# Kernel tuning notes

Measured on AMD Instinct MI355X. Metric: run time of the kernel, lower is better.

The kernel has to match this reference:

```python
import jax, jax.numpy as jnp
import numpy as np
from jax import lax


def conv2d(x, w, stride=1, padding=0, dilation=1, bias=None):
    s = (stride, stride) if isinstance(stride, int) else stride
    p = (padding, padding) if isinstance(padding, int) else padding
    d = (dilation, dilation) if isinstance(dilation, int) else dilation
    out = lax.conv_general_dilated(x, w, s, [(p[0], p[0]), (p[1], p[1])],
                                   rhs_dilation=d,
                                   dimension_numbers=('NCHW', 'OIHW', 'NCHW'))
    if bias is not None:
        out = out + bias[None, :, None, None]
    return out


def bn(x, eps=1e-5):
    # BatchNorm2d in training mode with default affine params (gamma=1, beta=0)
    m = x.mean((0, 2, 3), keepdims=True)
    v = jnp.mean((x - m) ** 2, (0, 2, 3), keepdims=True)
    return (x - m) * lax.rsqrt(v + eps)


def cbam(x, w_fc1, w_fc2, w_sp):
    mlp = lambda v: conv2d(jax.nn.relu(conv2d(v, w_fc1)), w_fc2)
    ca = jax.nn.sigmoid(mlp(x.mean((2, 3), keepdims=True)) + mlp(x.max((2, 3), keepdims=True)))
    x = x * ca
    sp = jnp.concatenate([x.mean(1, keepdims=True), x.max(1, keepdims=True)], 1)
    return x * jax.nn.sigmoid(conv2d(sp, w_sp, padding=3))


def deform_conv(x, offset, w_kernel, ks=3, padding=1):
    b, c, h, w = x.shape
    N = ks * ks
    # reorder interleaved offsets -> all x-offsets then all y-offsets
    reorder = jnp.concatenate([jnp.arange(0, 2 * N, 2), jnp.arange(1, 2 * N, 2)])
    offset = offset[:, reorder]
    xp = jnp.pad(x, ((0, 0), (0, 0), (padding, padding), (padding, padding)))
    Hp, Wp = h + 2 * padding, w + 2 * padding
    r = jnp.arange(-(ks - 1) // 2, (ks - 1) // 2 + 1)
    knx, kny = jnp.meshgrid(r, r, indexing='ij')
    p_n = jnp.concatenate([knx.ravel(), kny.ravel()]).astype(x.dtype).reshape(1, 2 * N, 1, 1)
    gx, gy = jnp.meshgrid(jnp.arange(1, h + 1), jnp.arange(1, w + 1), indexing='ij')
    p_0 = jnp.concatenate([jnp.broadcast_to(gx[None, None], (1, N, h, w)),
                           jnp.broadcast_to(gy[None, None], (1, N, h, w))], 1).astype(x.dtype)
    p = jnp.transpose(p_0 + p_n + offset, (0, 2, 3, 1))  # [b,h,w,2N]
    clampq = lambda q: jnp.concatenate([jnp.clip(q[..., :N], 0, Hp - 1),
                                        jnp.clip(q[..., N:], 0, Wp - 1)], -1)
    fl = jnp.floor(lax.stop_gradient(p))
    q_lt = clampq(fl).astype(jnp.int32)
    q_rb = clampq(fl + 1).astype(jnp.int32)
    q_lb = jnp.concatenate([q_lt[..., :N], q_rb[..., N:]], -1)
    q_rt = jnp.concatenate([q_rb[..., :N], q_lt[..., N:]], -1)
    mask = jnp.concatenate([(p[..., :N] < padding) | (p[..., :N] > Hp - 1 - padding),
                            (p[..., N:] < padding) | (p[..., N:] > Wp - 1 - padding)], -1)
    mask = lax.stop_gradient(mask.astype(p.dtype))
    # floor_p = p - (p - floor(p)) carries zero gradient in the original
    p = p * (1 - mask) + lax.stop_gradient(jnp.floor(p)) * mask
    p = clampq(p)
    px, py = p[..., :N], p[..., N:]
    def g(q, sx, sy):
        return ((1 + sx * (q[..., :N].astype(p.dtype) - px)) *
                (1 + sy * (q[..., N:].astype(p.dtype) - py)))
    xf = xp.reshape(b, c, Hp * Wp)
    def gather(q):
        idx = (q[..., :N] * Wp + q[..., N:]).reshape(b, 1, h * w * N)
        v = jnp.take_along_axis(xf, jnp.broadcast_to(idx, (b, c, h * w * N)), axis=2)
        return v.reshape(b, c, h, w, N)
    xo = (g(q_lt, 1, 1)[:, None] * gather(q_lt) + g(q_rb, -1, -1)[:, None] * gather(q_rb)
          + g(q_lb, 1, -1)[:, None] * gather(q_lb) + g(q_rt, -1, 1)[:, None] * gather(q_rt))
    # [b,c,h,w,N] -> [b,c,h*ks,w*ks] (N = kernel_row*ks + kernel_col)
    xo = xo.reshape(b, c, h, w, ks, ks).transpose(0, 1, 2, 4, 3, 5).reshape(b, c, h * ks, w * ks)
    return conv2d(xo, w_kernel, stride=ks)


def _forward(lf, hf, w_conv1_1, b_conv1_1, w_conv, w_offset, b_offset, w_deform,
             w_dil1, w_dil2, w_dil3, w_dil4, w_conv1, w_conv2,
             w_fc1, w_fc2, w_sp, w_conv1_2, b_conv1_2, w_conv3_3):
    hf = jax.nn.relu(bn(conv2d(hf, w_conv1_1, bias=b_conv1_1)))  # Conv1x1
    xc = jnp.split(lf, 4, axis=1)
    def branch(prev, extra, w_dil, dil):
        x = bn(conv2d(jnp.concatenate([prev, hf], 1), w_conv, padding=1))
        t = x + extra
        off = conv2d(t, w_offset, padding=1, bias=b_offset)
        d = deform_conv(t, off, w_deform)
        d = bn(conv2d(d, w_dil, padding=dil, dilation=dil))
        d = bn(conv2d(d, w_conv1, padding=1))
        d = cbam(d, w_fc1, w_fc2, w_sp)
        return bn(conv2d(d, w_conv2, padding=1))
    x0_1 = branch(xc[0], xc[1], w_dil1, 1)
    x1_2 = branch(x0_1, x0_1 + xc[2], w_dil2, 2)
    x2_3 = branch(x1_2, x1_2 + xc[3], w_dil3, 3)
    x3_4 = branch(x2_3, x2_3, w_dil4, 4)
    xx = jax.nn.relu(bn(conv2d(jnp.concatenate([x0_1, x1_2, x2_3, x3_4], 1),
                               w_conv1_2, bias=b_conv1_2)))
    return bn(conv2d(lf + xx, w_conv3_3, padding=1))


def setup_inputs() -> dict:
    key = jax.random.key(0)
    ks = jax.random.split(key, 20)
    B, C, H, W = 4, 64, 256, 256
    c4 = C // 4
    rn = lambda k, shp, s=0.05: jax.random.normal(k, shp, dtype=jnp.float32) * s
    return {
        'lf': rn(ks[0], (B, C, H, W), 1.0),
        'hf': rn(ks[1], (B, C, H, W), 1.0),
        'w_conv1_1': rn(ks[2], (c4, C, 1, 1)),
        'b_conv1_1': jnp.zeros((c4,), jnp.float32),
        'w_conv': rn(ks[3], (c4, C // 2, 3, 3)),
        'w_offset': rn(ks[4], (18, c4, 3, 3)),
        'b_offset': jnp.zeros((18,), jnp.float32),
        'w_deform': rn(ks[5], (c4, c4, 3, 3)),
        'w_dil1': rn(ks[6], (c4, c4, 3, 3)),
        'w_dil2': rn(ks[7], (c4, c4, 3, 3)),
        'w_dil3': rn(ks[8], (c4, c4, 3, 3)),
        'w_dil4': rn(ks[9], (c4, c4, 3, 3)),
        'w_conv1': rn(ks[10], (C, c4, 3, 3)),
        'w_conv2': rn(ks[11], (c4, C, 3, 3)),
        'w_fc1': rn(ks[12], (C // 16, C, 1, 1)),
        'w_fc2': rn(ks[13], (C, C // 16, 1, 1)),
        'w_sp': rn(ks[14], (1, 2, 7, 7)),
        'w_conv1_2': rn(ks[15], (C, C, 1, 1)),
        'b_conv1_2': jnp.zeros((C,), jnp.float32),
        'w_conv3_3': rn(ks[16], (C, C, 3, 3)),
    }


def reference(lf, hf, w_conv1_1, b_conv1_1, w_conv, w_offset, b_offset, w_deform,
              w_dil1, w_dil2, w_dil3, w_dil4, w_conv1, w_conv2,
              w_fc1, w_fc2, w_sp, w_conv1_2, b_conv1_2, w_conv3_3):
    return _forward(lf, hf, w_conv1_1, b_conv1_1, w_conv, w_offset, b_offset, w_deform,
                    w_dil1, w_dil2, w_dil3, w_dil4, w_conv1, w_conv2,
                    w_fc1, w_fc2, w_sp, w_conv1_2, b_conv1_2, w_conv3_3)
```

## Files before the change

kernel.cpp:

```cpp
#include <hip/hip_runtime.h>
#include <math.h>

#define HW 65536
#define Wd 256
#define Hd 256
#define Bn 4
#define NS 16

template<int CIN1,int CIN2,int COUT,int COB,int DIL>
__global__ __launch_bounds__(256) void conv3_k(
    const float* __restrict__ inA, long long a_bs,
    const float* __restrict__ inB,
    const float* __restrict__ add_in,
    const float* __restrict__ w, const float* __restrict__ bias,
    const float* __restrict__ scale_c, const float* __restrict__ scale_p,
    float* __restrict__ out)
{
    constexpr int CIN = CIN1 + CIN2;
    constexpr int SP = 2*DIL + 4;
    int tx = threadIdx.x & 15, ty = threadIdx.x >> 4;
    int j0 = blockIdx.x*64 + tx*4;
    int iy = blockIdx.y & 15;
    int chunk = blockIdx.y >> 4;
    int i = iy*16 + ty;
    int b = blockIdx.z;
    int o0 = chunk*COB;

    float acc[COB][4];
#pragma unroll
    for(int o=0;o<COB;o++){
        float bv = bias ? bias[o0+o] : 0.f;
#pragma unroll
        for(int q=0;q<4;q++) acc[o][q] = bv;
    }

    const float* spb = scale_p ? scale_p + (size_t)b*HW : nullptr;

    for(int c=0;c<CIN;c++){
        const float* cb;
        if (CIN2 == 0 || c < CIN1) cb = inA + (size_t)b*a_bs + (size_t)c*HW;
        else                       cb = inB + ((size_t)b*CIN2 + (c-CIN1))*HW;
        const float* ab = add_in ? add_in + (size_t)b*a_bs + (size_t)c*HW : nullptr;
        float sc = scale_c ? scale_c[b*CIN + c] : 1.f;

        float r[3][SP];
#pragma unroll
        for(int kh=0;kh<3;kh++){
#pragma unroll
            for(int t=0;t<SP;t++) r[kh][t] = 0.f;
            int ii = i + (kh-1)*DIL;
            if (ii < 0 || ii >= Hd) continue;
            const float* row = cb + ii*Wd;
            float4 c4 = *(const float4*)(row + j0);
            r[kh][DIL+0]=c4.x; r[kh][DIL+1]=c4.y; r[kh][DIL+2]=c4.z; r[kh][DIL+3]=c4.w;
#pragma unroll
            for(int t=0;t<DIL;t++){
                int jl = j0 - DIL + t;
                if (jl >= 0) r[kh][t] = row[jl];
                int jr = j0 + 4 + t;
                if (jr < Wd) r[kh][DIL+4+t] = row[jr];
            }
            if (ab){
                const float* arow = ab + ii*Wd;
                float4 a4 = *(const float4*)(arow + j0);
                r[kh][DIL+0]+=a4.x; r[kh][DIL+1]+=a4.y; r[kh][DIL+2]+=a4.z; r[kh][DIL+3]+=a4.w;
#pragma unroll
                for(int t=0;t<DIL;t++){
                    int jl = j0 - DIL + t;
                    if (jl >= 0) r[kh][t] += arow[jl];
                    int jr = j0 + 4 + t;
                    if (jr < Wd) r[kh][DIL+4+t] += arow[jr];
                }
            }
            if (spb){
                const float* srow = spb + ii*Wd;
                float4 s4 = *(const float4*)(srow + j0);
                r[kh][DIL+0]*=s4.x; r[kh][DIL+1]*=s4.y; r[kh][DIL+2]*=s4.z; r[kh][DIL+3]*=s4.w;
#pragma unroll
                for(int t=0;t<DIL;t++){
                    int jl = j0 - DIL + t;
                    if (jl >= 0) r[kh][t] *= srow[jl];
                    int jr = j0 + 4 + t;
                    if (jr < Wd) r[kh][DIL+4+t] *= srow[jr];
                }
            }
            if (scale_c){
#pragma unroll
                for(int t=0;t<SP;t++) r[kh][t] *= sc;
            }
        }

#pragma unroll
        for(int o=0;o<COB;o++){
#pragma unroll
            for(int kh=0;kh<3;kh++){
#pragma unroll
                for(int kw=0;kw<3;kw++){
                    float ww = w[((size_t)(o0+o)*CIN + c)*9 + kh*3 + kw];
#pragma unroll
                    for(int q=0;q<4;q++)
                        acc[o][q] = fmaf(ww, r[kh][kw*DIL + q], acc[o][q]);
                }
            }
        }
    }

    float* ob = out + ((size_t)b*COUT + o0)*HW + i*Wd + j0;
#pragma unroll
    for(int o=0;o<COB;o++){
        float4 v; v.x=acc[o][0]; v.y=acc[o][1]; v.z=acc[o][2]; v.w=acc[o][3];
        *(float4*)(ob + (size_t)o*HW) = v;
    }
}

template<int CIN,int COUT>
__global__ void conv1x1_k(const float* __restrict__ in, const float* __restrict__ w,
                          const float* __restrict__ bias, float* __restrict__ out)
{
    int p = blockIdx.x*256 + threadIdx.x;
    int b = blockIdx.y;
    const float* inb = in + (size_t)b*CIN*HW + p;
    float acc[COUT];
#pragma unroll
    for(int o=0;o<COUT;o++) acc[o] = bias ? bias[o] : 0.f;
    for(int c=0;c<CIN;c++){
        float v = inb[(size_t)c*HW];
#pragma unroll
        for(int o=0;o<COUT;o++) acc[o] += w[o*CIN+c]*v;
    }
    float* ob = out + (size_t)b*COUT*HW + p;
#pragma unroll
    for(int o=0;o<COUT;o++) ob[(size_t)o*HW] = acc[o];
}

__global__ void bn_stats_part(const float* __restrict__ x, int C, double* __restrict__ part)
{
    int c = blockIdx.x, s = blockIdx.y, tid = threadIdx.x;
    double sum = 0.0, sum2 = 0.0;
    for(int t=0;t<64;t++){
        int g = s*16384 + t*256 + tid;
        int b = g >> 16, p = g & 65535;
        double v = (double)x[((size_t)b*C + c)*HW + p];
        sum += v; sum2 += v*v;
    }
    __shared__ double sh[512];
    sh[tid] = sum; sh[256+tid] = sum2;
    __syncthreads();
    for(int o=128;o>0;o>>=1){
        if (tid < o){ sh[tid] += sh[tid+o]; sh[256+tid] += sh[256+tid+o]; }
        __syncthreads();
    }
    if (tid==0){ part[(c*NS+s)*2] = sh[0]; part[(c*NS+s)*2+1] = sh[256]; }
}

__global__ void bn_finalize(const double* __restrict__ part, int C, float* __restrict__ mr)
{
    int c = threadIdx.x;
    if (c >= C) return;
    double s = 0.0, s2 = 0.0;
    for(int k=0;k<NS;k++){ s += part[(c*NS+k)*2]; s2 += part[(c*NS+k)*2+1]; }
    double n = (double)Bn*HW;
    double m = s/n;
    double var = s2/n - m*m;
    mr[c]   = (float)m;
    mr[C+c] = rsqrtf((float)var + 1e-5f);
}

__global__ void bn_apply_k(const float* __restrict__ x, const float* __restrict__ mr, int C,
                           const float* __restrict__ e1, long long e1_bs,
                           const float* __restrict__ e2, long long e2_bs,
                           float* __restrict__ out, int relu)
{
    int p = (blockIdx.x*256 + threadIdx.x)*4;
    int c = blockIdx.y, b = blockIdx.z;
    size_t idx = ((size_t)b*C + c)*HW + p;
    float m = mr[c], r = mr[C+c];
    float4 v = *(const float4*)(x + idx);
    v.x = (v.x-m)*r; v.y = (v.y-m)*r; v.z = (v.z-m)*r; v.w = (v.w-m)*r;
    if (e1){
        float4 a = *(const float4*)(e1 + (size_t)b*e1_bs + (size_t)c*HW + p);
        v.x+=a.x; v.y+=a.y; v.z+=a.z; v.w+=a.w;
    }
    if (e2){
        float4 a = *(const float4*)(e2 + (size_t)b*e2_bs + (size_t)c*HW + p);
        v.x+=a.x; v.y+=a.y; v.z+=a.z; v.w+=a.w;
    }
    if (relu){
        v.x=fmaxf(v.x,0.f); v.y=fmaxf(v.y,0.f); v.z=fmaxf(v.z,0.f); v.w=fmaxf(v.w,0.f);
    }
    *(float4*)(out + idx) = v;
}

__global__ void cat4_k(const float* __restrict__ x0, const float* __restrict__ x1,
                       const float* __restrict__ x2, const float* __restrict__ x3,
                       float* __restrict__ out)
{
    int p = (blockIdx.x*256 + threadIdx.x)*4;
    int c = blockIdx.y, b = blockIdx.z;
    const float* src = (c<16)? x0 : (c<32)? x1 : (c<48)? x2 : x3;
    *(float4*)(out + ((size_t)b*64 + c)*HW + p) =
        *(const float4*)(src + ((size_t)b*16 + (c&15))*HW + p);
}

__global__ void deform_k(const float* __restrict__ t, const float* __restrict__ off,
                         const float* __restrict__ w, float* __restrict__ out)
{
    int tx = threadIdx.x & 15, ty = threadIdx.x >> 4;
    int j = blockIdx.x*16 + tx;
    int i = blockIdx.y*16 + ty;
    int b = blockIdx.z;
    const float* tb = t + (size_t)b*16*HW;
    const float* ob = off + (size_t)b*18*HW + i*Wd + j;
    float acc[16];
#pragma unroll
    for(int o=0;o<16;o++) acc[o] = 0.f;

    for(int n=0;n<9;n++){
        float offx = ob[(size_t)(2*n)*HW];
        float offy = ob[(size_t)(2*n+1)*HW];
        float px = (float)(i + n/3) + offx;
        float py = (float)(j + n%3) + offy;
        float flx = floorf(px), fly = floorf(py);
        float qltx = fminf(fmaxf(flx,       0.f), 257.f);
        float qlty = fminf(fmaxf(fly,       0.f), 257.f);
        float qrbx = fminf(fmaxf(flx + 1.f, 0.f), 257.f);
        float qrby = fminf(fmaxf(fly + 1.f, 0.f), 257.f);
        if (px < 1.f || px > 256.f) px = flx;
        if (py < 1.f || py > 256.f) py = fly;
        px = fminf(fmaxf(px, 0.f), 257.f);
        py = fminf(fmaxf(py, 0.f), 257.f);
        float wx_lt = 1.f + (qltx - px);
        float wx_rb = 1.f - (qrbx - px);
        float wy_lt = 1.f + (qlty - py);
        float wy_rb = 1.f - (qrby - py);
        float glt = wx_lt*wy_lt, grb = wx_rb*wy_rb, glb = wx_lt*wy_rb, grt = wx_rb*wy_lt;
        int ix0 = (int)qltx - 1, iy0 = (int)qlty - 1;
        int ix1 = (int)qrbx - 1, iy1 = (int)qrby - 1;
        bool vx0 = (ix0>=0 && ix0<Hd), vx1 = (ix1>=0 && ix1<Hd);
        bool vy0 = (iy0>=0 && iy0<Wd), vy1 = (iy1>=0 && iy1<Wd);
        int i00 = ix0*Wd+iy0, i01 = ix0*Wd+iy1, i10 = ix1*Wd+iy0, i11 = ix1*Wd+iy1;
        float vals[16];
#pragma unroll
        for(int c=0;c<16;c++){
            const float* tc = tb + (size_t)c*HW;
            float v00 = (vx0&&vy0) ? tc[i00] : 0.f;
            float v11 = (vx1&&vy1) ? tc[i11] : 0.f;
            float v01 = (vx0&&vy1) ? tc[i01] : 0.f;
            float v10 = (vx1&&vy0) ? tc[i10] : 0.f;
            vals[c] = glt*v00 + grb*v11 + glb*v01 + grt*v10;
        }
#pragma unroll
        for(int o=0;o<16;o++){
            float a = acc[o];
#pragma unroll
            for(int c=0;c<16;c++) a += w[(o*16+c)*9 + n] * vals[c];
            acc[o] = a;
        }
    }
    float* outb = out + (size_t)b*16*HW + i*Wd + j;
#pragma unroll
    for(int o=0;o<16;o++) outb[(size_t)o*HW] = acc[o];
}

__global__ void pool_k(const float* __restrict__ x, float* __restrict__ pavg, float* __restrict__ pmax)
{
    int bc = blockIdx.x;
    int tid = threadIdx.x;
    const float* p = x + (size_t)bc*HW;
    float s = 0.f, mx = -1e30f;
    for(int i=tid;i<HW;i+=256){ float v = p[i]; s += v; mx = fmaxf(mx, v); }
    __shared__ float sh[512];
    sh[tid] = s; sh[256+tid] = mx;
    __syncthreads();
    for(int o=128;o>0;o>>=1){
        if (tid < o){ sh[tid] += sh[tid+o]; sh[256+tid] = fmaxf(sh[256+tid], sh[256+tid+o]); }
        __syncthreads();
    }
    if (tid==0){ pavg[bc] = sh[0] / (float)HW; pmax[bc] = sh[256]; }
}

__global__ void ca_k(const float* __restrict__ pavg, const float* __restrict__ pmax,
                     const float* __restrict__ w1, const float* __restrict__ w2,
                     float* __restrict__ ca)
{
    int b = blockIdx.x;
    int tid = threadIdx.x;
    __shared__ float ha[4], hm[4];
    if (tid < 4){
        float sa = 0.f, sm = 0.f;
        for(int c=0;c<64;c++){
            sa += w1[tid*64+c] * pavg[b*64+c];
            sm += w1[tid*64+c] * pmax[b*64+c];
        }
        ha[tid] = fmaxf(sa, 0.f);
        hm[tid] = fmaxf(sm, 0.f);
    }
    __syncthreads();
    float s = 0.f;
    for(int h=0;h<4;h++) s += w2[tid*4+h] * (ha[h] + hm[h]);
    ca[b*64+tid] = 1.f / (1.f + expf(-s));
}

__global__ void spstats_k(const float* __restrict__ x, const float* __restrict__ ca,
                          float* __restrict__ spm, float* __restrict__ spx)
{
    int p = blockIdx.x*256 + threadIdx.x;
    int b = blockIdx.y;
    const float* xb = x + (size_t)b*64*HW + p;
    const float* cb = ca + b*64;
    float s = 0.f, mx = -1e30f;
    for(int c=0;c<64;c++){
        float v = xb[(size_t)c*HW] * cb[c];
        s += v; mx = fmaxf(mx, v);
    }
    spm[(size_t)b*HW+p] = s * (1.f/64.f);
    spx[(size_t)b*HW+p] = mx;
}

__global__ void spconv_k(const float* __restrict__ spm, const float* __restrict__ spx,
                         const float* __restrict__ wsp, float* __restrict__ sa)
{
    int tx = threadIdx.x & 15, ty = threadIdx.x >> 4;
    int j = blockIdx.x*16 + tx;
    int i = blockIdx.y*16 + ty;
    int b = blockIdx.z;
    const float* m = spm + (size_t)b*HW;
    const float* x = spx + (size_t)b*HW;
    float s = 0.f;
    for(int kh=0;kh<7;kh++){
        int ii = i + kh - 3; if (ii<0||ii>=Hd) continue;
        for(int kw=0;kw<7;kw++){
            int jj = j + kw - 3; if (jj<0||jj>=Wd) continue;
            s += wsp[kh*7+kw]*m[ii*Wd+jj] + wsp[49+kh*7+kw]*x[ii*Wd+jj];
        }
    }
    sa[(size_t)b*HW + i*Wd + j] = 1.f / (1.f + expf(-s));
}

extern "C" void kernel_launch(void* const* d_in, const int* in_sizes, int n_in,
                              void* d_out, int out_size, void* d_ws, size_t ws_size,
                              hipStream_t stream)
{
    const float* lf        = (const float*)d_in[0];
    const float* hf        = (const float*)d_in[1];
    const float* w_conv1_1 = (const float*)d_in[2];
    const float* b_conv1_1 = (const float*)d_in[3];
    const float* w_conv    = (const float*)d_in[4];
    const float* w_offset  = (const float*)d_in[5];
    const float* b_offset  = (const float*)d_in[6];
    const float* w_deform  = (const float*)d_in[7];
    const float* w_dil[4]  = {(const float*)d_in[8],(const float*)d_in[9],
                              (const float*)d_in[10],(const float*)d_in[11]};
    const float* w_conv1   = (const float*)d_in[12];
    const float* w_conv2   = (const float*)d_in[13];
    const float* w_fc1     = (const float*)d_in[14];
    const float* w_fc2     = (const float*)d_in[15];
    const float* w_sp      = (const float*)d_in[16];
    const float* w_conv1_2 = (const float*)d_in[17];
    const float* b_conv1_2 = (const float*)d_in[18];
    const float* w_conv3_3 = (const float*)d_in[19];
    float* out = (float*)d_out;

    float* ws = (float*)d_ws;
    size_t off_f = 0;
    auto alloc = [&](size_t n){ float* p = ws + off_f; off_f += n; return p; };
    const size_t S16 = (size_t)Bn*16*HW;

    float* hf_p  = alloc(S16);
    float* B16_0 = alloc(S16);
    float* B16_1 = alloc(S16);
    float* B16_2 = alloc(S16);
    float* B64F  = ws;
    float* Boff  = alloc((size_t)Bn*18*HW);
    float* B64_0 = alloc((size_t)Bn*64*HW);
    float* xk[4] = {alloc(S16),alloc(S16),alloc(S16),alloc(S16)};
    float* spm   = alloc((size_t)Bn*HW);
    float* spx   = alloc((size_t)Bn*HW);
    float* sa    = alloc((size_t)Bn*HW);
    float* mr    = alloc(128);
    float* pavg  = alloc(256);
    float* pmax  = alloc(256);
    float* ca    = alloc(256);
    double* part = (double*)alloc(64*NS*2*2);
    (void)ws_size; (void)in_sizes; (void)n_in; (void)out_size;

    dim3 blk(256);
    dim3 gpix(HW/256, Bn);
    dim3 gtile(16,16,Bn);
    dim3 gapply16(HW/1024,16,Bn), gapply64(HW/1024,64,Bn);
    const long long bs16 = 16LL*HW, bs64 = 64LL*HW;

    auto bn_stats = [&](const float* x, int C){
        bn_stats_part<<<dim3(C,NS),blk,0,stream>>>(x, C, part);
        bn_finalize<<<1,64,0,stream>>>(part, C, mr);
    };

    conv1x1_k<64,16><<<gpix,blk,0,stream>>>(hf, w_conv1_1, b_conv1_1, hf_p);
    bn_stats(hf_p, 16);
    bn_apply_k<<<gapply16,blk,0,stream>>>(hf_p, mr, 16, nullptr,0, nullptr,0, hf_p, 1);

    for(int k=0;k<4;k++){
        const float* prev; long long prev_bs;
        if (k==0){ prev = lf;      prev_bs = bs64; }
        else     { prev = xk[k-1]; prev_bs = bs16; }
        conv3_k<16,16,16,16,1><<<dim3(4,16,Bn),blk,0,stream>>>(
            prev, prev_bs, hf_p, nullptr, w_conv, nullptr, nullptr, nullptr, B16_0);
        bn_stats(B16_0, 16);
        const float* e1; long long e1bs; const float* e2 = nullptr; long long e2bs = 0;
        if (k==0){ e1 = lf + 16*HW; e1bs = bs64; }
        else if (k==3){ e1 = xk[2]; e1bs = bs16; }
        else { e1 = xk[k-1]; e1bs = bs16; e2 = lf + (size_t)(k+1)*16*HW; e2bs = bs64; }
        bn_apply_k<<<gapply16,blk,0,stream>>>(B16_0, mr, 16, e1,e1bs, e2,e2bs, B16_0, 0);
        conv3_k<16,0,18,18,1><<<dim3(4,16,Bn),blk,0,stream>>>(
            B16_0, bs16, nullptr, nullptr, w_offset, b_offset, nullptr, nullptr, Boff);
        deform_k<<<gtile,blk,0,stream>>>(B16_0, Boff, w_deform, B16_1);
        switch(k){
        case 0: conv3_k<16,0,16,16,1><<<dim3(4,16,Bn),blk,0,stream>>>(B16_1, bs16, nullptr, nullptr, w_dil[0], nullptr, nullptr, nullptr, B16_2); break;
        case 1: conv3_k<16,0,16,16,2><<<dim3(4,16,Bn),blk,0,stream>>>(B16_1, bs16, nullptr, nullptr, w_dil[1], nullptr, nullptr, nullptr, B16_2); break;
        case 2: conv3_k<16,0,16,16,3><<<dim3(4,16,Bn),blk,0,stream>>>(B16_1, bs16, nullptr, nullptr, w_dil[2], nullptr, nullptr, nullptr, B16_2); break;
        case 3: conv3_k<16,0,16,16,4><<<dim3(4,16,Bn),blk,0,stream>>>(B16_1, bs16, nullptr, nullptr, w_dil[3], nullptr, nullptr, nullptr, B16_2); break;
        }
        bn_stats(B16_2, 16);
        bn_apply_k<<<gapply16,blk,0,stream>>>(B16_2, mr, 16, nullptr,0, nullptr,0, B16_2, 0);
        conv3_k<16,0,64,16,1><<<dim3(4,64,Bn),blk,0,stream>>>(
            B16_2, bs16, nullptr, nullptr, w_conv1, nullptr, nullptr, nullptr, B64_0);
        bn_stats(B64_0, 64);
        bn_apply_k<<<gapply64,blk,0,stream>>>(B64_0, mr, 64, nullptr,0, nullptr,0, B64_0, 0);
        pool_k<<<Bn*64,blk,0,stream>>>(B64_0, pavg, pmax);
        ca_k<<<Bn,dim3(64),0,stream>>>(pavg, pmax, w_fc1, w_fc2, ca);
        spstats_k<<<dim3(256,Bn),blk,0,stream>>>(B64_0, ca, spm, spx);
        spconv_k<<<gtile,blk,0,stream>>>(spm, spx, w_sp, sa);
        conv3_k<64,0,16,16,1><<<dim3(4,16,Bn),blk,0,stream>>>(
            B64_0, bs64, nullptr, nullptr, w_conv2, nullptr, ca, sa, B16_1);
        bn_stats(B16_1, 16);
        bn_apply_k<<<gapply16,blk,0,stream>>>(B16_1, mr, 16, nullptr,0, nullptr,0, xk[k], 0);
    }

    cat4_k<<<dim3(HW/1024,64,Bn),blk,0,stream>>>(xk[0], xk[1], xk[2], xk[3], B64F);
    conv1x1_k<64,64><<<gpix,blk,0,stream>>>(B64F, w_conv1_2, b_conv1_2, B64_0);
    bn_stats(B64_0, 64);
    bn_apply_k<<<gapply64,blk,0,stream>>>(B64_0, mr, 64, nullptr,0, nullptr,0, B64_0, 1);
    conv3_k<64,0,64,16,1><<<dim3(4,64,Bn),blk,0,stream>>>(
        lf, bs64, nullptr, B64_0, w_conv3_3, nullptr, nullptr, nullptr, B64F);
    bn_stats(B64F, 64);
    bn_apply_k<<<gapply64,blk,0,stream>>>(B64F, mr, 64, nullptr,0, nullptr,0, out, 0);
}
```

Baseline: 4.301 ms.

## Stage 3x3 conv input tiles with halos in shared memory per channel group

Replaces the register-based 3x3 conv, where each thread loaded its own rows plus halo from global memory for four pixels, with a version that stages a 4-row by 72-column input tile (halo included) for four channels at a time in LDS. Each thread then computes one pixel across all output channels of its chunk. The spatial attention map is also staged once in LDS, and the grids grow to cover the 4-row groups. The aim is to cut redundant, unaligned global halo loads. The trade-offs are extra barriers and less reuse of each weight, now one FMA per weight load instead of four.

```diff
diff --git a/kernel.cpp b/kernel.cpp
--- a/kernel.cpp
+++ b/kernel.cpp
@@ -8,7 +8,7 @@
 #define NS 16
 
 template<int CIN1,int CIN2,int COUT,int COB,int DIL>
-__global__ __launch_bounds__(256) void conv3_k(
+__global__ __launch_bounds__(256) void conv3s_k(
     const float* __restrict__ inA, long long a_bs,
     const float* __restrict__ inB,
     const float* __restrict__ add_in,
@@ -17,100 +17,99 @@
     float* __restrict__ out)
 {
     constexpr int CIN = CIN1 + CIN2;
-    constexpr int SP = 2*DIL + 4;
-    int tx = threadIdx.x & 15, ty = threadIdx.x >> 4;
-    int j0 = blockIdx.x*64 + tx*4;
-    int iy = blockIdx.y & 15;
-    int chunk = blockIdx.y >> 4;
-    int i = iy*16 + ty;
-    int b = blockIdx.z;
-    int o0 = chunk*COB;
-
-    float acc[COB][4];
-#pragma unroll
-    for(int o=0;o<COB;o++){
-        float bv = bias ? bias[o0+o] : 0.f;
-#pragma unroll
-        for(int q=0;q<4;q++) acc[o][q] = bv;
-    }
-
-    const float* spb = scale_p ? scale_p + (size_t)b*HW : nullptr;
-
-    for(int c=0;c<CIN;c++){
-        const float* cb;
-        if (CIN2 == 0 || c < CIN1) cb = inA + (size_t)b*a_bs + (size_t)c*HW;
-        else                       cb = inB + ((size_t)b*CIN2 + (c-CIN1))*HW;
-        const float* ab = add_in ? add_in + (size_t)b*a_bs + (size_t)c*HW : nullptr;
-        float sc = scale_c ? scale_c[b*CIN + c] : 1.f;
-
-        float r[3][SP];
-#pragma unroll
-        for(int kh=0;kh<3;kh++){
-#pragma unroll
-            for(int t=0;t<SP;t++) r[kh][t] = 0.f;
-            int ii = i + (kh-1)*DIL;
-            if (ii < 0 || ii >= Hd) continue;
-            const float* row = cb + ii*Wd;
-            float4 c4 = *(const float4*)(row + j0);
-            r[kh][DIL+0]=c4.x; r[kh][DIL+1]=c4.y; r[kh][DIL+2]=c4.z; r[kh][DIL+3]=c4.w;
-#pragma unroll
-            for(int t=0;t<DIL;t++){
-                int jl = j0 - DIL + t;
-                if (jl >= 0) r[kh][t] = row[jl];
-                int jr = j0 + 4 + t;
-                if (jr < Wd) r[kh][DIL+4+t] = row[jr];
-            }
-            if (ab){
-                const float* arow = ab + ii*Wd;
-                float4 a4 = *(const float4*)(arow + j0);
-                r[kh][DIL+0]+=a4.x; r[kh][DIL+1]+=a4.y; r[kh][DIL+2]+=a4.z; r[kh][DIL+3]+=a4.w;
-#pragma unroll
-                for(int t=0;t<DIL;t++){
-                    int jl = j0 - DIL + t;
-                    if (jl >= 0) r[kh][t] += arow[jl];
-                    int jr = j0 + 4 + t;
-                    if (jr < Wd) r[kh][DIL+4+t] += arow[jr];
+    constexpr int R   = 4 + 2*DIL;
+    constexpr int CG  = 4;
+    constexpr int F4  = 18;
+    __shared__ float lds[CG][R][72];
+    __shared__ float lsp[R][72];
+
+    int tid = threadIdx.x;
+    int tx = tid & 63, ty = tid >> 6;
+    int j0 = blockIdx.x * 64;
+    constexpr int NCH = COUT / COB;
+    int chunk = blockIdx.y % NCH;
+    int rg    = blockIdx.y / NCH;
+    int i0 = rg * 4;
+    int b  = blockIdx.z;
+    int o0 = chunk * COB;
+
+    float spv[9];
+    if (scale_p){
+        const float* spb = scale_p + (size_t)b*HW;
+        for (int idx = tid; idx < R*F4; idx += 256){
+            int f4 = idx % F4, row = idx / F4;
+            int ii = i0 - DIL + row;
+            int c0 = j0 - 4 + f4*4;
+            float4 v = {0.f,0.f,0.f,0.f};
+            if (ii >= 0 && ii < Hd && c0 >= 0 && c0 < Wd)
+                v = *(const float4*)(spb + ii*Wd + c0);
+            *(float4*)&lsp[row][f4*4] = v;
+        }
+        __syncthreads();
+#pragma unroll
+        for (int kh=0;kh<3;kh++)
+#pragma unroll
+        for (int kw=0;kw<3;kw++)
+            spv[kh*3+kw] = lsp[ty + DIL + (kh-1)*DIL][tx + 4 + (kw-1)*DIL];
+    }
+
+    float acc[COB];
+#pragma unroll
+    for (int o=0;o<COB;o++) acc[o] = bias ? bias[o0+o] : 0.f;
+
+    for (int cg0 = 0; cg0 < CIN; cg0 += CG){
+        __syncthreads();
+        for (int idx = tid; idx < CG*R*F4; idx += 256){
+            int f4  = idx % F4;
+            int row = (idx / F4) % R;
+            int cc  = idx / (F4*R);
+            int c   = cg0 + cc;
+            int ii  = i0 - DIL + row;
+            int c0  = j0 - 4 + f4*4;
+            float4 v = {0.f,0.f,0.f,0.f};
+            if (ii >= 0 && ii < Hd && c0 >= 0 && c0 < Wd){
+                const float* cb = (CIN2 == 0 || c < CIN1)
+                    ? inA + (size_t)b*a_bs + (size_t)c*HW
+                    : inB + ((size_t)b*CIN2 + (c-CIN1))*HW;
+                v = *(const float4*)(cb + ii*Wd + c0);
+                if (add_in){
+                    float4 a = *(const float4*)(add_in + (size_t)b*a_bs + (size_t)c*HW + ii*Wd + c0);
+                    v.x+=a.x; v.y+=a.y; v.z+=a.z; v.w+=a.w;
                 }
             }
-            if (spb){
-                const float* srow = spb + ii*Wd;
-                float4 s4 = *(const float4*)(srow + j0);
-                r[kh][DIL+0]*=s4.x; r[kh][DIL+1]*=s4.y; r[kh][DIL+2]*=s4.z; r[kh][DIL+3]*=s4.w;
-#pragma unroll
-                for(int t=0;t<DIL;t++){
-                    int jl = j0 - DIL + t;
-                    if (jl >= 0) r[kh][t] *= srow[jl];
-                    int jr = j0 + 4 + t;
-                    if (jr < Wd) r[kh][DIL+4+t] *= srow[jr];
-                }
+            *(float4*)&lds[cc][row][f4*4] = v;
+        }
+        __syncthreads();
+#pragma unroll
+        for (int cc=0; cc<CG; cc++){
+            int c = cg0 + cc;
+            float v[9];
+#pragma unroll
+            for (int kh=0;kh<3;kh++)
+#pragma unroll
+            for (int kw=0;kw<3;kw++)
+                v[kh*3+kw] = lds[cc][ty + DIL + (kh-1)*DIL][tx + 4 + (kw-1)*DIL];
+            if (scale_p){
+#pragma unroll
+                for (int t=0;t<9;t++) v[t] *= spv[t];
             }
             if (scale_c){
-#pragma unroll
-                for(int t=0;t<SP;t++) r[kh][t] *= sc;
+                float sc = scale_c[b*CIN + c];
+#pragma unroll
+                for (int t=0;t<9;t++) v[t] *= sc;
             }
-        }
-
-#pragma unroll
-        for(int o=0;o<COB;o++){
-#pragma unroll
-            for(int kh=0;kh<3;kh++){
-#pragma unroll
-                for(int kw=0;kw<3;kw++){
-                    float ww = w[((size_t)(o0+o)*CIN + c)*9 + kh*3 + kw];
-#pragma unroll
-                    for(int q=0;q<4;q++)
-                        acc[o][q] = fmaf(ww, r[kh][kw*DIL + q], acc[o][q]);
-                }
+#pragma unroll
+            for (int o=0;o<COB;o++){
+                const float* wp = w + ((size_t)(o0+o)*CIN + c)*9;
+#pragma unroll
+                for (int t=0;t<9;t++) acc[o] = fmaf(wp[t], v[t], acc[o]);
             }
         }
     }
 
-    float* ob = out + ((size_t)b*COUT + o0)*HW + i*Wd + j0;
-#pragma unroll
-    for(int o=0;o<COB;o++){
-        float4 v; v.x=acc[o][0]; v.y=acc[o][1]; v.z=acc[o][2]; v.w=acc[o][3];
-        *(float4*)(ob + (size_t)o*HW) = v;
-    }
+    float* ob = out + ((size_t)b*COUT + o0)*HW + (i0+ty)*Wd + j0 + tx;
+#pragma unroll
+    for (int o=0;o<COB;o++) ob[(size_t)o*HW] = acc[o];
 }
 
 template<int CIN,int COUT>
@@ -387,6 +386,8 @@
     dim3 blk(256);
     dim3 gpix(HW/256, Bn);
     dim3 gtile(16,16,Bn);
+    dim3 gc16(4,64,Bn);
+    dim3 gc64(4,256,Bn);
     dim3 gapply16(HW/1024,16,Bn), gapply64(HW/1024,64,Bn);
     const long long bs16 = 16LL*HW, bs64 = 64LL*HW;
 
@@ -403,7 +404,7 @@
         const float* prev; long long prev_bs;
         if (k==0){ prev = lf;      prev_bs = bs64; }
         else     { prev = xk[k-1]; prev_bs = bs16; }
-        conv3_k<16,16,16,16,1><<<dim3(4,16,Bn),blk,0,stream>>>(
+        conv3s_k<16,16,16,16,1><<<gc16,blk,0,stream>>>(
             prev, prev_bs, hf_p, nullptr, w_conv, nullptr, nullptr, nullptr, B16_0);
         bn_stats(B16_0, 16);
         const float* e1; long long e1bs; const float* e2 = nullptr; long long e2bs = 0;
@@ -411,18 +412,18 @@
         else if (k==3){ e1 = xk[2]; e1bs = bs16; }
         else { e1 = xk[k-1]; e1bs = bs16; e2 = lf + (size_t)(k+1)*16*HW; e2bs = bs64; }
         bn_apply_k<<<gapply16,blk,0,stream>>>(B16_0, mr, 16, e1,e1bs, e2,e2bs, B16_0, 0);
-        conv3_k<16,0,18,18,1><<<dim3(4,16,Bn),blk,0,stream>>>(
+        conv3s_k<16,0,18,18,1><<<gc16,blk,0,stream>>>(
             B16_0, bs16, nullptr, nullptr, w_offset, b_offset, nullptr, nullptr, Boff);
         deform_k<<<gtile,blk,0,stream>>>(B16_0, Boff, w_deform, B16_1);
         switch(k){
-        case 0: conv3_k<16,0,16,16,1><<<dim3(4,16,Bn),blk,0,stream>>>(B16_1, bs16, nullptr, nullptr, w_dil[0], nullptr, nullptr, nullptr, B16_2); break;
-        case 1: conv3_k<16,0,16,16,2><<<dim3(4,16,Bn),blk,0,stream>>>(B16_1, bs16, nullptr, nullptr, w_dil[1], nullptr, nullptr, nullptr, B16_2); break;
-        case 2: conv3_k<16,0,16,16,3><<<dim3(4,16,Bn),blk,0,stream>>>(B16_1, bs16, nullptr, nullptr, w_dil[2], nullptr, nullptr, nullptr, B16_2); break;
-        case 3: conv3_k<16,0,16,16,4><<<dim3(4,16,Bn),blk,0,stream>>>(B16_1, bs16, nullptr, nullptr, w_dil[3], nullptr, nullptr, nullptr, B16_2); break;
+        case 0: conv3s_k<16,0,16,16,1><<<gc16,blk,0,stream>>>(B16_1, bs16, nullptr, nullptr, w_dil[0], nullptr, nullptr, nullptr, B16_2); break;
+        case 1: conv3s_k<16,0,16,16,2><<<gc16,blk,0,stream>>>(B16_1, bs16, nullptr, nullptr, w_dil[1], nullptr, nullptr, nullptr, B16_2); break;
+        case 2: conv3s_k<16,0,16,16,3><<<gc16,blk,0,stream>>>(B16_1, bs16, nullptr, nullptr, w_dil[2], nullptr, nullptr, nullptr, B16_2); break;
+        case 3: conv3s_k<16,0,16,16,4><<<gc16,blk,0,stream>>>(B16_1, bs16, nullptr, nullptr, w_dil[3], nullptr, nullptr, nullptr, B16_2); break;
         }
         bn_stats(B16_2, 16);
         bn_apply_k<<<gapply16,blk,0,stream>>>(B16_2, mr, 16, nullptr,0, nullptr,0, B16_2, 0);
-        conv3_k<16,0,64,16,1><<<dim3(4,64,Bn),blk,0,stream>>>(
+        conv3s_k<16,0,64,16,1><<<gc64,blk,0,stream>>>(
             B16_2, bs16, nullptr, nullptr, w_conv1, nullptr, nullptr, nullptr, B64_0);
         bn_stats(B64_0, 64);
         bn_apply_k<<<gapply64,blk,0,stream>>>(B64_0, mr, 64, nullptr,0, nullptr,0, B64_0, 0);
@@ -430,7 +431,7 @@
         ca_k<<<Bn,dim3(64),0,stream>>>(pavg, pmax, w_fc1, w_fc2, ca);
         spstats_k<<<dim3(256,Bn),blk,0,stream>>>(B64_0, ca, spm, spx);
         spconv_k<<<gtile,blk,0,stream>>>(spm, spx, w_sp, sa);
-        conv3_k<64,0,16,16,1><<<dim3(4,16,Bn),blk,0,stream>>>(
+        conv3s_k<64,0,16,16,1><<<gc16,blk,0,stream>>>(
             B64_0, bs64, nullptr, nullptr, w_conv2, nullptr, ca, sa, B16_1);
         bn_stats(B16_1, 16);
         bn_apply_k<<<gapply16,blk,0,stream>>>(B16_1, mr, 16, nullptr,0, nullptr,0, xk[k], 0);
@@ -440,7 +441,7 @@
     conv1x1_k<64,64><<<gpix,blk,0,stream>>>(B64F, w_conv1_2, b_conv1_2, B64_0);
     bn_stats(B64_0, 64);
     bn_apply_k<<<gapply64,blk,0,stream>>>(B64_0, mr, 64, nullptr,0, nullptr,0, B64_0, 1);
-    conv3_k<64,0,64,16,1><<<dim3(4,64,Bn),blk,0,stream>>>(
+    conv3s_k<64,0,64,16,1><<<gc64,blk,0,stream>>>(
         lf, bs64, nullptr, B64_0, w_conv3_3, nullptr, nullptr, nullptr, B64F);
     bn_stats(B64F, 64);
     bn_apply_k<<<gapply64,blk,0,stream>>>(B64F, mr, 64, nullptr,0, nullptr,0, out, 0);
```

New measurement: 4.586 ms. +6.6%, slower.

## Split conv3 input channels across thread groups with shared-memory reduction

Applied to the files above, without the earlier changes.

The 3x3 conv kernel now splits the input-channel loop across KZ thread groups in each block, with each group covering fewer rows (TH). Partial sums are combined through a serialized shared-memory reduction before the store. The grid grows so more blocks are in flight, which is meant to improve occupancy and latency hiding on these small-grid convolutions. The spatial scale map is also loaded once per thread instead of once per channel. The cost is extra shared memory, several __syncthreads barriers, and less halo reuse per block.

```diff
diff --git a/kernel.cpp b/kernel.cpp
--- a/kernel.cpp
+++ b/kernel.cpp
@@ -7,8 +7,8 @@
 #define Bn 4
 #define NS 16
 
-template<int CIN1,int CIN2,int COUT,int COB,int DIL>
-__global__ __launch_bounds__(256) void conv3_k(
+template<int CIN1,int CIN2,int COUT,int COB,int DIL,int KZ,int TH>
+__global__ __launch_bounds__(256) void conv3r_k(
     const float* __restrict__ inA, long long a_bs,
     const float* __restrict__ inB,
     const float* __restrict__ add_in,
@@ -17,31 +17,59 @@
     float* __restrict__ out)
 {
     constexpr int CIN = CIN1 + CIN2;
-    constexpr int SP = 2*DIL + 4;
-    int tx = threadIdx.x & 15, ty = threadIdx.x >> 4;
-    int j0 = blockIdx.x*64 + tx*4;
-    int iy = blockIdx.y & 15;
-    int chunk = blockIdx.y >> 4;
-    int i = iy*16 + ty;
-    int b = blockIdx.z;
-    int o0 = chunk*COB;
+    constexpr int CPG = CIN / KZ;
+    constexpr int SP  = 2*DIL + 4;
+    constexpr int NCH = COUT / COB;
+    __shared__ float red[COB][64*TH];
+
+    int tid = threadIdx.x;
+    int kz  = tid / (16*TH);
+    int r2  = tid % (16*TH);
+    int tx  = r2 & 15, ty = r2 >> 4;
+    int j0  = blockIdx.x*64 + tx*4;
+    int chunk = blockIdx.y % NCH;
+    int rg    = blockIdx.y / NCH;
+    int i  = rg*TH + ty;
+    int b  = blockIdx.z;
+    int o0 = chunk * COB;
+
+    float sw[3][SP];
+    if (scale_p){
+        const float* spb = scale_p + (size_t)b*HW;
+#pragma unroll
+        for(int kh=0;kh<3;kh++){
+#pragma unroll
+            for(int t=0;t<SP;t++) sw[kh][t] = 0.f;
+            int ii = i + (kh-1)*DIL;
+            if (ii < 0 || ii >= Hd) continue;
+            const float* row = spb + ii*Wd;
+            float4 c4 = *(const float4*)(row + j0);
+            sw[kh][DIL+0]=c4.x; sw[kh][DIL+1]=c4.y; sw[kh][DIL+2]=c4.z; sw[kh][DIL+3]=c4.w;
+#pragma unroll
+            for(int t=0;t<DIL;t++){
+                int jl = j0 - DIL + t;
+                if (jl >= 0) sw[kh][t] = row[jl];
+                int jr = j0 + 4 + t;
+                if (jr < Wd) sw[kh][DIL+4+t] = row[jr];
+            }
+        }
+    }
 
     float acc[COB][4];
 #pragma unroll
     for(int o=0;o<COB;o++){
-        float bv = bias ? bias[o0+o] : 0.f;
+        float bv = (kz==0 && bias) ? bias[o0+o] : 0.f;
 #pragma unroll
         for(int q=0;q<4;q++) acc[o][q] = bv;
     }
 
-    const float* spb = scale_p ? scale_p + (size_t)b*HW : nullptr;
-
-    for(int c=0;c<CIN;c++){
+    int c0 = kz * CPG;
+    for(int cc=0; cc<CPG; cc++){
+        int c = c0 + cc;
         const float* cb;
         if (CIN2 == 0 || c < CIN1) cb = inA + (size_t)b*a_bs + (size_t)c*HW;
         else                       cb = inB + ((size_t)b*CIN2 + (c-CIN1))*HW;
         const float* ab = add_in ? add_in + (size_t)b*a_bs + (size_t)c*HW : nullptr;
-        float sc = scale_c ? scale_c[b*CIN + c] : 1.f;
 
         float r[3][SP];
 #pragma unroll
@@ -72,44 +100,62 @@
                     if (jr < Wd) r[kh][DIL+4+t] += arow[jr];
                 }
             }
-            if (spb){
-                const float* srow = spb + ii*Wd;
-                float4 s4 = *(const float4*)(srow + j0);
-                r[kh][DIL+0]*=s4.x; r[kh][DIL+1]*=s4.y; r[kh][DIL+2]*=s4.z; r[kh][DIL+3]*=s4.w;
-#pragma unroll
-                for(int t=0;t<DIL;t++){
-                    int jl = j0 - DIL + t;
-                    if (jl >= 0) r[kh][t] *= srow[jl];
-                    int jr = j0 + 4 + t;
-                    if (jr < Wd) r[kh][DIL+4+t] *= srow[jr];
-                }
+        }
+        if (scale_p){
+#pragma unroll
+            for(int kh=0;kh<3;kh++)
+#pragma unroll
+            for(int t=0;t<SP;t++) r[kh][t] *= sw[kh][t];
+        }
+        if (scale_c){
+            float sc = scale_c[b*CIN + c];
+#pragma unroll
+            for(int kh=0;kh<3;kh++)
+#pragma unroll
+            for(int t=0;t<SP;t++) r[kh][t] *= sc;
+        }
+
+#pragma unroll
+        for(int o=0;o<COB;o++){
+            const float* wp = w + ((size_t)(o0+o)*CIN + c)*9;
+#pragma unroll
+            for(int kh=0;kh<3;kh++)
+#pragma unroll
+            for(int kw=0;kw<3;kw++){
+                float ww = wp[kh*3+kw];
+#pragma unroll
+                for(int q=0;q<4;q++)
+                    acc[o][q] = fmaf(ww, r[kh][kw*DIL + q], acc[o][q]);
             }
-            if (scale_c){
-#pragma unroll
-                for(int t=0;t<SP;t++) r[kh][t] *= sc;
+        }
+    }
+
+    int pl = ty*64 + tx*4;
+    if (kz == 0){
+#pragma unroll
+        for(int o=0;o<COB;o++){
+            float4 v; v.x=acc[o][0]; v.y=acc[o][1]; v.z=acc[o][2]; v.w=acc[o][3];
+            *(float4*)&red[o][pl] = v;
+        }
+    }
+    __syncthreads();
+#pragma unroll
+    for(int g=1; g<KZ; g++){
+        if (kz == g){
+#pragma unroll
+            for(int o=0;o<COB;o++){
+                float4 v = *(float4*)&red[o][pl];
+                v.x+=acc[o][0]; v.y+=acc[o][1]; v.z+=acc[o][2]; v.w+=acc[o][3];
+                *(float4*)&red[o][pl] = v;
             }
         }
-
-#pragma unroll
-        for(int o=0;o<COB;o++){
-#pragma unroll
-            for(int kh=0;kh<3;kh++){
-#pragma unroll
-                for(int kw=0;kw<3;kw++){
-                    float ww = w[((size_t)(o0+o)*CIN + c)*9 + kh*3 + kw];
-#pragma unroll
-                    for(int q=0;q<4;q++)
-                        acc[o][q] = fmaf(ww, r[kh][kw*DIL + q], acc[o][q]);
-                }
-            }
-        }
-    }
-
-    float* ob = out + ((size_t)b*COUT + o0)*HW + i*Wd + j0;
-#pragma unroll
-    for(int o=0;o<COB;o++){
-        float4 v; v.x=acc[o][0]; v.y=acc[o][1]; v.z=acc[o][2]; v.w=acc[o][3];
-        *(float4*)(ob + (size_t)o*HW) = v;
+        __syncthreads();
+    }
+    if (kz == 0){
+        float* ob = out + ((size_t)b*COUT + o0)*HW + i*Wd + j0;
+#pragma unroll
+        for(int o=0;o<COB;o++)
+            *(float4*)(ob + (size_t)o*HW) = *(float4*)&red[o][pl];
     }
 }
 
@@ -387,6 +433,10 @@
     dim3 blk(256);
     dim3 gpix(HW/256, Bn);
     dim3 gtile(16,16,Bn);
+    dim3 g16(4,32,Bn);
+    dim3 g16x4(4,128,Bn);
+    dim3 g64(4,64,Bn);
+    dim3 g64x4(4,256,Bn);
     dim3 gapply16(HW/1024,16,Bn), gapply64(HW/1024,64,Bn);
     const long long bs16 = 16LL*HW, bs64 = 64LL*HW;
 
@@ -403,7 +453,7 @@
         const float* prev; long long prev_bs;
         if (k==0){ prev = lf;      prev_bs = bs64; }
         else     { prev = xk[k-1]; prev_bs = bs16; }
-        conv3_k<16,16,16,16,1><<<dim3(4,16,Bn),blk,0,stream>>>(
+        conv3r_k<16,16,16,16,1,2,8><<<g16,blk,0,stream>>>(
             prev, prev_bs, hf_p, nullptr, w_conv, nullptr, nullptr, nullptr, B16_0);
         bn_stats(B16_0, 16);
         const float* e1; long long e1bs; const float* e2 = nullptr; long long e2bs = 0;
@@ -411,18 +461,18 @@
         else if (k==3){ e1 = xk[2]; e1bs = bs16; }
         else { e1 = xk[k-1]; e1bs = bs16; e2 = lf + (size_t)(k+1)*16*HW; e2bs = bs64; }
         bn_apply_k<<<gapply16,blk,0,stream>>>(B16_0, mr, 16, e1,e1bs, e2,e2bs, B16_0, 0);
-        conv3_k<16,0,18,18,1><<<dim3(4,16,Bn),blk,0,stream>>>(
+        conv3r_k<16,0,18,18,1,2,8><<<g16,blk,0,stream>>>(
             B16_0, bs16, nullptr, nullptr, w_offset, b_offset, nullptr, nullptr, Boff);
         deform_k<<<gtile,blk,0,stream>>>(B16_0, Boff, w_deform, B16_1);
         switch(k){
-        case 0: conv3_k<16,0,16,16,1><<<dim3(4,16,Bn),blk,0,stream>>>(B16_1, bs16, nullptr, nullptr, w_dil[0], nullptr, nullptr, nullptr, B16_2); break;
-        case 1: conv3_k<16,0,16,16,2><<<dim3(4,16,Bn),blk,0,stream>>>(B16_1, bs16, nullptr, nullptr, w_dil[1], nullptr, nullptr, nullptr, B16_2); break;
-        case 2: conv3_k<16,0,16,16,3><<<dim3(4,16,Bn),blk,0,stream>>>(B16_1, bs16, nullptr, nullptr, w_dil[2], nullptr, nullptr, nullptr, B16_2); break;
-        case 3: conv3_k<16,0,16,16,4><<<dim3(4,16,Bn),blk,0,stream>>>(B16_1, bs16, nullptr, nullptr, w_dil[3], nullptr, nullptr, nullptr, B16_2); break;
+        case 0: conv3r_k<16,0,16,16,1,2,8><<<g16,blk,0,stream>>>(B16_1, bs16, nullptr, nullptr, w_dil[0], nullptr, nullptr, nullptr, B16_2); break;
+        case 1: conv3r_k<16,0,16,16,2,2,8><<<g16,blk,0,stream>>>(B16_1, bs16, nullptr, nullptr, w_dil[1], nullptr, nullptr, nullptr, B16_2); break;
+        case 2: conv3r_k<16,0,16,16,3,2,8><<<g16,blk,0,stream>>>(B16_1, bs16, nullptr, nullptr, w_dil[2], nullptr, nullptr, nullptr, B16_2); break;
+        case 3: conv3r_k<16,0,16,16,4,2,8><<<g16,blk,0,stream>>>(B16_1, bs16, nullptr, nullptr, w_dil[3], nullptr, nullptr, nullptr, B16_2); break;
         }
         bn_stats(B16_2, 16);
         bn_apply_k<<<gapply16,blk,0,stream>>>(B16_2, mr, 16, nullptr,0, nullptr,0, B16_2, 0);
-        conv3_k<16,0,64,16,1><<<dim3(4,64,Bn),blk,0,stream>>>(
+        conv3r_k<16,0,64,16,1,2,8><<<g16x4,blk,0,stream>>>(
             B16_2, bs16, nullptr, nullptr, w_conv1, nullptr, nullptr, nullptr, B64_0);
         bn_stats(B64_0, 64);
         bn_apply_k<<<gapply64,blk,0,stream>>>(B64_0, mr, 64, nullptr,0, nullptr,0, B64_0, 0);
@@ -430,7 +480,7 @@
         ca_k<<<Bn,dim3(64),0,stream>>>(pavg, pmax, w_fc1, w_fc2, ca);
         spstats_k<<<dim3(256,Bn),blk,0,stream>>>(B64_0, ca, spm, spx);
         spconv_k<<<gtile,blk,0,stream>>>(spm, spx, w_sp, sa);
-        conv3_k<64,0,16,16,1><<<dim3(4,16,Bn),blk,0,stream>>>(
+        conv3r_k<64,0,16,16,1,4,4><<<g64,blk,0,stream>>>(
             B64_0, bs64, nullptr, nullptr, w_conv2, nullptr, ca, sa, B16_1);
         bn_stats(B16_1, 16);
         bn_apply_k<<<gapply16,blk,0,stream>>>(B16_1, mr, 16, nullptr,0, nullptr,0, xk[k], 0);
@@ -440,7 +490,7 @@
     conv1x1_k<64,64><<<gpix,blk,0,stream>>>(B64F, w_conv1_2, b_conv1_2, B64_0);
     bn_stats(B64_0, 64);
     bn_apply_k<<<gapply64,blk,0,stream>>>(B64_0, mr, 64, nullptr,0, nullptr,0, B64_0, 1);
-    conv3_k<64,0,64,16,1><<<dim3(4,64,Bn),blk,0,stream>>>(
+    conv3r_k<64,0,64,16,1,4,4><<<g64x4,blk,0,stream>>>(
         lf, bs64, nullptr, B64_0, w_conv3_3, nullptr, nullptr, nullptr, B64F);
     bn_stats(B64F, 64);
     bn_apply_k<<<gapply64,blk,0,stream>>>(B64F, mr, 64, nullptr,0, nullptr,0, out, 0);
```

After: 4.317 ms. No clear change (+0.4%).
